# Kernel tuning notes

Hardware: AMD Instinct MI355X
Metric: run time of the kernel (lower is better)

The kernel has to match this reference:

```python
import jax, jax.numpy as jnp
import numpy as np

B, S, DIM = 32, 1, 4096
HQ, HKV, HD = 32, 8, 128
MAX_SEQ = 2048
START_POS = 2047


def _apply_rope(t, cos, sin):
    # t: [B, S, H, HD]; cos/sin: [S, HD//2]; interleaved complex rotation (Llama style)
    b, s, h, d = t.shape
    t = t.reshape(b, s, h, d // 2, 2)
    t0, t1 = t[..., 0], t[..., 1]
    c = cos[None, :, None, :]
    sn = sin[None, :, None, :]
    out = jnp.stack([t0 * c - t1 * sn, t0 * sn + t1 * c], axis=-1)
    return out.reshape(b, s, h, d)


def setup_inputs() -> dict:
    key = jax.random.key(0)
    ks = jax.random.split(key, 8)
    w_scale = 0.02
    x = jax.random.normal(ks[0], (B, S, DIM), dtype=jnp.float32)
    wq = jax.random.normal(ks[1], (HQ * HD, DIM), dtype=jnp.float32) * w_scale
    wk = jax.random.normal(ks[2], (HKV * HD, DIM), dtype=jnp.float32) * w_scale
    wv = jax.random.normal(ks[3], (HKV * HD, DIM), dtype=jnp.float32) * w_scale
    wo = jax.random.normal(ks[4], (HQ * HD, DIM), dtype=jnp.float32).T * w_scale
    wo = jnp.asarray(wo)  # [DIM, HQ*HD] as torch Linear weight [out,in]
    cache_k = jax.random.normal(ks[5], (B, MAX_SEQ, HKV, HD), dtype=jnp.float32)
    cache_v = jax.random.normal(ks[6], (B, MAX_SEQ, HKV, HD), dtype=jnp.float32)
    # rotary frequencies for the current position(s)
    inv_freq = 1.0 / (10000.0 ** (np.arange(0, HD, 2, dtype=np.float32) / HD))  # [HD//2]
    pos = np.arange(START_POS, START_POS + S, dtype=np.float32)[:, None]  # [S,1]
    ang = pos * inv_freq[None, :]
    freqs_cos = jnp.asarray(np.cos(ang), dtype=jnp.float32)
    freqs_sin = jnp.asarray(np.sin(ang), dtype=jnp.float32)
    return {"x": x, "wq": wq, "wk": wk, "wv": wv, "wo": wo,
            "cache_k": cache_k, "cache_v": cache_v,
            "freqs_cos": freqs_cos, "freqs_sin": freqs_sin,
            "start_pos": START_POS}


def reference(x, wq, wk, wv, wo, cache_k, cache_v, freqs_cos, freqs_sin, start_pos):
    b, s, dim = x.shape
    hd = 2 * freqs_cos.shape[-1]
    hq = wq.shape[0] // hd
    hkv = wk.shape[0] // hd
    n_rep = hq // hkv

    # QKV projections (torch Linear: y = x @ W.T)
    xq = (x @ wq.T).reshape(b, s, hq, hd)
    xk = (x @ wk.T).reshape(b, s, hkv, hd)
    xv = (x @ wv.T).reshape(b, s, hkv, hd)

    # RoPE on q and k
    xq = _apply_rope(xq, freqs_cos, freqs_sin)
    xk = _apply_rope(xk, freqs_cos, freqs_sin)

    # KV cache update at start_pos (static python int -> static slicing)
    ck = jax.lax.dynamic_update_slice(cache_k, xk, (0, start_pos, 0, 0))
    cv = jax.lax.dynamic_update_slice(cache_v, xv, (0, start_pos, 0, 0))
    t = start_pos + s
    keys = ck[:, :t]    # [B, T, HKV, HD]
    values = cv[:, :t]  # [B, T, HKV, HD]

    # Grouped attention without materializing repeated KV (repeat_kv fused into einsum)
    q = xq.reshape(b, s, hkv, n_rep, hd)
    scores = jnp.einsum('bsgrd,btgd->bgrst', q, keys) / jnp.sqrt(jnp.asarray(hd, x.dtype))
    attn = jax.nn.softmax(scores, axis=-1)  # decode step: attends to full history, no mask
    out = jnp.einsum('bgrst,btgd->bsgrd', attn, values).reshape(b, s, hq * hd)
    return out @ wo.T  # [B, S, DIM]
```

## Files before the change

kernel.cpp:

```cpp
#include <hip/hip_runtime.h>
#include <hip/hip_bf16.h>

typedef float vf4 __attribute__((ext_vector_type(4)));

#define B_    32
#define DIM_  4096
#define TSEQ  2048
#define LASTT 2047
#define NCH   32
#define CHUNK 64
#define CSTR  528
#define RSTR  132
#define SCL   0.08838834764831845f
#define KCH   256
#define ROWS1 6144
#define ROWS4 4096

__device__ __forceinline__ float dotv(vf4 a, vf4 b) {
    return fmaf(a[0], b[0], fmaf(a[1], b[1], fmaf(a[2], b[2], a[3] * b[3])));
}

__device__ __forceinline__ void gemm_tile_part(
    const float* __restrict__ W, const float* __restrict__ X,
    float* __restrict__ part, int rloc_base, int grow_base,
    int kb0, int kc, int rowsTot) {
    __shared__ __align__(16) vf4 wS[128][17];
    __shared__ __align__(16) vf4 xS[16][33];
    const int tid = threadIdx.x;
    const int rg = tid >> 3, bg = tid & 7;
    const int sr4 = tid >> 4, swf = tid & 15;
    const int sb = tid >> 3, sxf = tid & 7;
    float c[4][4] = {};

    for (int tile = 0; tile < 4; ++tile) {
        const int kb4 = (kb0 + tile * 64) >> 2;
        #pragma unroll
        for (int jj = 0; jj < 8; ++jj) {
            const int row = sr4 + 16 * jj;
            wS[row][swf] = __builtin_nontemporal_load(
                ((const vf4*)(W + (size_t)(rloc_base + row) * DIM_)) + kb4 + swf);
        }
        #pragma unroll
        for (int jj = 0; jj < 2; ++jj) {
            const int f4i = sxf + 8 * jj;
            xS[f4i][sb] = ((const vf4*)(X + (size_t)sb * DIM_))[kb4 + f4i];
        }
        __syncthreads();
        #pragma unroll
        for (int k4 = 0; k4 < 16; ++k4) {
            const vf4 w0 = wS[rg      ][k4];
            const vf4 w1 = wS[rg + 32 ][k4];
            const vf4 w2 = wS[rg + 64 ][k4];
            const vf4 w3 = wS[rg + 96 ][k4];
            const vf4 x0 = xS[k4][bg     ];
            const vf4 x1 = xS[k4][bg + 8 ];
            const vf4 x2 = xS[k4][bg + 16];
            const vf4 x3 = xS[k4][bg + 24];
            #pragma unroll
            for (int cm = 0; cm < 4; ++cm) {
                c[0][0] = fmaf(w0[cm], x0[cm], c[0][0]);
                c[0][1] = fmaf(w0[cm], x1[cm], c[0][1]);
                c[0][2] = fmaf(w0[cm], x2[cm], c[0][2]);
                c[0][3] = fmaf(w0[cm], x3[cm], c[0][3]);
                c[1][0] = fmaf(w1[cm], x0[cm], c[1][0]);
                c[1][1] = fmaf(w1[cm], x1[cm], c[1][1]);
                c[1][2] = fmaf(w1[cm], x2[cm], c[1][2]);
                c[1][3] = fmaf(w1[cm], x3[cm], c[1][3]);
                c[2][0] = fmaf(w2[cm], x0[cm], c[2][0]);
                c[2][1] = fmaf(w2[cm], x1[cm], c[2][1]);
                c[2][2] = fmaf(w2[cm], x2[cm], c[2][2]);
                c[2][3] = fmaf(w2[cm], x3[cm], c[2][3]);
                c[3][0] = fmaf(w3[cm], x0[cm], c[3][0]);
                c[3][1] = fmaf(w3[cm], x1[cm], c[3][1]);
                c[3][2] = fmaf(w3[cm], x2[cm], c[3][2]);
                c[3][3] = fmaf(w3[cm], x3[cm], c[3][3]);
            }
        }
        __syncthreads();
    }
    float* pb = part + (size_t)kc * rowsTot * 32;
    #pragma unroll
    for (int i = 0; i < 4; ++i)
        #pragma unroll
        for (int j = 0; j < 4; ++j)
            pb[(size_t)(grow_base + rg + 32 * i) * 32 + bg + 8 * j] = c[i][j];
}

__global__ __launch_bounds__(256) void k1_qkv(
    const float* __restrict__ x,  const float* __restrict__ wq,
    const float* __restrict__ wk, const float* __restrict__ wv,
    float* __restrict__ part) {
    const int rb = blockIdx.x >> 4, kc = blockIdx.x & 15;
    const int rbase = rb * 128;
    const float* W; int rloc;
    if (rbase < 4096)      { W = wq; rloc = rbase; }
    else if (rbase < 5120) { W = wk; rloc = rbase - 4096; }
    else                   { W = wv; rloc = rbase - 5120; }
    gemm_tile_part(W, x, part, rloc, rbase, kc * KCH, kc, ROWS1);
}

__global__ __launch_bounds__(256) void k1b_comb(
    const float* __restrict__ part, const float* __restrict__ fcos,
    const float* __restrict__ fsin, float* __restrict__ q_ws,
    float* __restrict__ k_ws, float* __restrict__ v_ws) {
    const int tid = threadIdx.x;
    const int b = tid & 31;
    const int row0 = (blockIdx.x * 8 + (tid >> 5)) * 2;
    float e = 0.f, o = 0.f;
    #pragma unroll
    for (int kc = 0; kc < 16; ++kc) {
        const float* pb = part + (size_t)kc * (ROWS1 * 32);
        e += pb[(size_t)row0 * 32 + b];
        o += pb[(size_t)(row0 + 1) * 32 + b];
    }
    if (row0 < 5120) {
        const int d = row0 & 127;
        const float cj = fcos[d >> 1], sj = fsin[d >> 1];
        const float re = e * cj - o * sj;
        const float ro = e * sj + o * cj;
        if (row0 < 4096) {
            q_ws[(size_t)b * 4096 + row0]     = re * SCL;
            q_ws[(size_t)b * 4096 + row0 + 1] = ro * SCL;
        } else {
            k_ws[(size_t)b * 1024 + row0 - 4096] = re;
            k_ws[(size_t)b * 1024 + row0 - 4095] = ro;
        }
    } else {
        v_ws[(size_t)b * 1024 + row0 - 5120] = e;
        v_ws[(size_t)b * 1024 + row0 - 5119] = o;
    }
}

__global__ __launch_bounds__(64) void k2_attn(
    const float* __restrict__ q_ws, const float* __restrict__ k_ws,
    const float* __restrict__ v_ws, const float* __restrict__ cK,
    const float* __restrict__ cV,   float* __restrict__ cws) {
    __shared__ float p_lds[4][64];
    const int blk = blockIdx.x;
    const int b = blk >> 8, g = (blk >> 5) & 7, c = blk & 31;
    const int lane = threadIdx.x & 63;
    const int tbase = c * CHUNK;
    const int s = lane & 7, pown = lane >> 3;

    const vf4* qb4 = (const vf4*)(q_ws + ((size_t)b * 32 + g * 4) * 128);
    vf4 q4[4][4];
    #pragma unroll
    for (int r = 0; r < 4; ++r)
        #pragma unroll
        for (int j = 0; j < 4; ++j)
            q4[r][j] = qb4[r * 32 + j * 8 + s];

    const vf4* kwsrow = (const vf4*)(k_ws + ((size_t)b * 8 + g) * 128);
    const vf4* vwsrow = (const vf4*)(v_ws + ((size_t)b * 8 + g) * 128);

    vf4 kb[4];
    {
        const int t = tbase + pown;
        const vf4* kr = (t == LASTT) ? kwsrow
            : (const vf4*)(cK + (((size_t)b * TSEQ + t) * 8 + g) * 128);
        #pragma unroll
        for (int j = 0; j < 4; ++j)
            kb[j] = __builtin_nontemporal_load(&kr[j * 8 + s]);
    }
    #pragma unroll
    for (int pg = 0; pg < 8; ++pg) {
        vf4 kn[4];
        if (pg < 7) {
            const int t = tbase + (pg + 1) * 8 + pown;
            const vf4* kr = (t == LASTT) ? kwsrow
                : (const vf4*)(cK + (((size_t)b * TSEQ + t) * 8 + g) * 128);
            #pragma unroll
            for (int j = 0; j < 4; ++j)
                kn[j] = __builtin_nontemporal_load(&kr[j * 8 + s]);
        }
        float a0 = 0.f, a1 = 0.f, a2 = 0.f, a3 = 0.f;
        #pragma unroll
        for (int j = 0; j < 4; ++j) {
            a0 += dotv(q4[0][j], kb[j]);
            a1 += dotv(q4[1][j], kb[j]);
            a2 += dotv(q4[2][j], kb[j]);
            a3 += dotv(q4[3][j], kb[j]);
        }
        #pragma unroll
        for (int m = 4; m >= 1; m >>= 1) {
            a0 += __shfl_xor(a0, m); a1 += __shfl_xor(a1, m);
            a2 += __shfl_xor(a2, m); a3 += __shfl_xor(a3, m);
        }
        const int idx = pg * 8 + pown;
        if (s == 0) p_lds[0][idx] = a0;
        if (s == 1) p_lds[1][idx] = a1;
        if (s == 2) p_lds[2][idx] = a2;
        if (s == 3) p_lds[3][idx] = a3;
        #pragma unroll
        for (int j = 0; j < 4; ++j) kb[j] = kn[j];
    }
    __syncthreads();

    const int h = lane >> 5, col = lane & 31;
    vf4 vb;
    {
        const int t = tbase + h;
        const vf4* vp = (t == LASTT) ? vwsrow
            : (const vf4*)(cV + (((size_t)b * TSEQ + t) * 8 + g) * 128);
        vb = __builtin_nontemporal_load(&vp[col]);
    }

    float sc[4], M[4], S[4];
    #pragma unroll
    for (int r = 0; r < 4; ++r) sc[r] = p_lds[r][lane];
    #pragma unroll
    for (int r = 0; r < 4; ++r) {
        float m = sc[r];
        #pragma unroll
        for (int msk = 32; msk >= 1; msk >>= 1) m = fmaxf(m, __shfl_xor(m, msk));
        M[r] = m;
        const float p = __expf(sc[r] - m);
        p_lds[r][lane] = p;
        float su = p;
        #pragma unroll
        for (int msk = 32; msk >= 1; msk >>= 1) su += __shfl_xor(su, msk);
        S[r] = su;
    }
    __syncthreads();

    float a[4][4] = {};
    #pragma unroll 8
    for (int tt = 0; tt < 32; ++tt) {
        vf4 vn;
        if (tt < 31) {
            const int t = tbase + (tt + 1) * 2 + h;
            const vf4* vp = (t == LASTT) ? vwsrow
                : (const vf4*)(cV + (((size_t)b * TSEQ + t) * 8 + g) * 128);
            vn = __builtin_nontemporal_load(&vp[col]);
        }
        #pragma unroll
        for (int r = 0; r < 4; ++r) {
            const float pr = p_lds[r][tt * 2 + h];
            a[r][0] = fmaf(pr, vb[0], a[r][0]);
            a[r][1] = fmaf(pr, vb[1], a[r][1]);
            a[r][2] = fmaf(pr, vb[2], a[r][2]);
            a[r][3] = fmaf(pr, vb[3], a[r][3]);
        }
        vb = vn;
    }
    #pragma unroll
    for (int r = 0; r < 4; ++r)
        #pragma unroll
        for (int j = 0; j < 4; ++j) a[r][j] += __shfl_xor(a[r][j], 32);

    float* base = cws + (size_t)blk * CSTR;
    if (lane < 32) {
        #pragma unroll
        for (int r = 0; r < 4; ++r) {
            vf4 v; v[0] = a[r][0]; v[1] = a[r][1]; v[2] = a[r][2]; v[3] = a[r][3];
            *(vf4*)(base + r * RSTR + col * 4) = v;
        }
    }
    if (lane == 0) {
        #pragma unroll
        for (int r = 0; r < 4; ++r) {
            base[r * RSTR + 128] = M[r];
            base[r * RSTR + 129] = S[r];
        }
    }
}

__global__ __launch_bounds__(256) void k3_comb(const float* __restrict__ cws,
                                               float* __restrict__ attn) {
    const int blk = blockIdx.x;
    const int b = blk >> 3, g = blk & 7;
    const int tid = threadIdx.x, r = tid >> 6, lane = tid & 63;
    const float* base0 = cws + (size_t)blk * 32 * CSTR + r * RSTR;
    float mi[32], si[32];
    float Mg = -3.4e38f;
    #pragma unroll
    for (int ci = 0; ci < 32; ++ci) {
        mi[ci] = base0[(size_t)ci * CSTR + 128];
        si[ci] = base0[(size_t)ci * CSTR + 129];
        Mg = fmaxf(Mg, mi[ci]);
    }
    float w[32], Sg = 0.f;
    #pragma unroll
    for (int ci = 0; ci < 32; ++ci) {
        w[ci] = __expf(mi[ci] - Mg);
        Sg = fmaf(si[ci], w[ci], Sg);
    }
    const float inv = 1.f / Sg;
    #pragma unroll
    for (int dd = 0; dd < 2; ++dd) {
        const int d = lane + dd * 64;
        float o = 0.f;
        #pragma unroll
        for (int ci = 0; ci < 32; ++ci)
            o = fmaf(base0[(size_t)ci * CSTR + d], w[ci], o);
        attn[((size_t)b * 32 + g * 4 + r) * 128 + d] = o * inv;
    }
}

__global__ __launch_bounds__(256) void k4_out(
    const float* __restrict__ attn, const float* __restrict__ wo,
    float* __restrict__ part) {
    const int rb = blockIdx.x >> 4, kc = blockIdx.x & 15;
    const int rbase = rb * 128;
    gemm_tile_part(wo, attn, part, rbase, rbase, kc * KCH, kc, ROWS4);
}

__global__ __launch_bounds__(256) void k4b_comb(const float* __restrict__ part,
                                                float* __restrict__ out) {
    const int tid = threadIdx.x;
    const int b = tid & 31;
    const int row = blockIdx.x * 8 + (tid >> 5);
    float acc = 0.f;
    #pragma unroll
    for (int kc = 0; kc < 16; ++kc)
        acc += part[(size_t)kc * (ROWS4 * 32) + (size_t)row * 32 + b];
    out[(size_t)b * 4096 + row] = acc;
}

extern "C" void kernel_launch(void* const* d_in, const int* in_sizes, int n_in,
                              void* d_out, int out_size, void* d_ws, size_t ws_size,
                              hipStream_t stream) {
    const float* x    = (const float*)d_in[0];
    const float* wq   = (const float*)d_in[1];
    const float* wk   = (const float*)d_in[2];
    const float* wv   = (const float*)d_in[3];
    const float* wo   = (const float*)d_in[4];
    const float* cK   = (const float*)d_in[5];
    const float* cV   = (const float*)d_in[6];
    const float* fcos = (const float*)d_in[7];
    const float* fsin = (const float*)d_in[8];
    float* ws   = (float*)d_ws;
    float* A    = ws;
    float* q_ws = ws + 4325376;
    float* k_ws = ws + 4456448;
    float* v_ws = ws + 4489216;
    float* attn = ws + 4521984;
    float* out  = (float*)d_out;

    hipLaunchKernelGGL(k1_qkv,   dim3(768),  dim3(256), 0, stream,
                       x, wq, wk, wv, A);
    hipLaunchKernelGGL(k1b_comb, dim3(384),  dim3(256), 0, stream,
                       A, fcos, fsin, q_ws, k_ws, v_ws);
    hipLaunchKernelGGL(k2_attn,  dim3(8192), dim3(64),  0, stream,
                       q_ws, k_ws, v_ws, cK, cV, A);
    hipLaunchKernelGGL(k3_comb,  dim3(256),  dim3(256), 0, stream, A, attn);
    hipLaunchKernelGGL(k4_out,   dim3(512),  dim3(256), 0, stream, attn, wo, A);
    hipLaunchKernelGGL(k4b_comb, dim3(512),  dim3(256), 0, stream, A, out);
}
```

Baseline: 186.8 us.

## Restructure attention split: per-batch chunk blocks covering all KV heads with contiguous rows

The attention kernel now launches one 256-thread block per batch and 128-token chunk, where each wave walks 32 tokens and lanes split across all 8 KV heads. Each K/V cache row is therefore read as one contiguous 4 KB segment instead of per-head strided pieces. Softmax partials are reduced across waves in LDS, and a single record per (batch, chunk) is written, which halves the number of partials the combine kernel merges. Separately, the weight loads in the GEMM tile drop the nontemporal hint. The costs are more LDS, extra barriers and fewer, larger blocks (512 instead of 8192).

```diff
diff --git a/kernel.cpp b/kernel.cpp
--- a/kernel.cpp
+++ b/kernel.cpp
@@ -7,14 +7,11 @@
 #define DIM_  4096
 #define TSEQ  2048
 #define LASTT 2047
-#define NCH   32
-#define CHUNK 64
-#define CSTR  528
-#define RSTR  132
 #define SCL   0.08838834764831845f
 #define KCH   256
 #define ROWS1 6144
 #define ROWS4 4096
+#define RECF  4224
 
 __device__ __forceinline__ float dotv(vf4 a, vf4 b) {
     return fmaf(a[0], b[0], fmaf(a[1], b[1], fmaf(a[2], b[2], a[3] * b[3])));
@@ -37,8 +34,8 @@
         #pragma unroll
         for (int jj = 0; jj < 8; ++jj) {
             const int row = sr4 + 16 * jj;
-            wS[row][swf] = __builtin_nontemporal_load(
-                ((const vf4*)(W + (size_t)(rloc_base + row) * DIM_)) + kb4 + swf);
+            wS[row][swf] =
+                ((const vf4*)(W + (size_t)(rloc_base + row) * DIM_))[kb4 + swf];
         }
         #pragma unroll
         for (int jj = 0; jj < 2; ++jj) {
@@ -131,16 +128,20 @@
     }
 }
 
-__global__ __launch_bounds__(64) void k2_attn(
+__global__ __launch_bounds__(256) void k2_attn(
     const float* __restrict__ q_ws, const float* __restrict__ k_ws,
     const float* __restrict__ v_ws, const float* __restrict__ cK,
     const float* __restrict__ cV,   float* __restrict__ cws) {
-    __shared__ float p_lds[4][64];
+    __shared__ float p_lds[8][4][129];
+    __shared__ __align__(16) float pacc[4][8][132];
+    __shared__ float wred[4][32];
+    __shared__ float wsum[4][32];
+    __shared__ float mM[32];
     const int blk = blockIdx.x;
-    const int b = blk >> 8, g = (blk >> 5) & 7, c = blk & 31;
-    const int lane = threadIdx.x & 63;
-    const int tbase = c * CHUNK;
-    const int s = lane & 7, pown = lane >> 3;
+    const int b = blk >> 4, ch = blk & 15;
+    const int tid = threadIdx.x, wave = tid >> 6, lane = tid & 63;
+    const int g = lane >> 3, s = lane & 7;
+    const int tb = ch * 128 + wave * 32;
 
     const vf4* qb4 = (const vf4*)(q_ws + ((size_t)b * 32 + g * 4) * 128);
     vf4 q4[4][4];
@@ -155,18 +156,18 @@
 
     vf4 kb[4];
     {
-        const int t = tbase + pown;
+        const int t = tb;
         const vf4* kr = (t == LASTT) ? kwsrow
             : (const vf4*)(cK + (((size_t)b * TSEQ + t) * 8 + g) * 128);
         #pragma unroll
         for (int j = 0; j < 4; ++j)
             kb[j] = __builtin_nontemporal_load(&kr[j * 8 + s]);
     }
-    #pragma unroll
-    for (int pg = 0; pg < 8; ++pg) {
+    #pragma unroll 4
+    for (int tt = 0; tt < 32; ++tt) {
         vf4 kn[4];
-        if (pg < 7) {
-            const int t = tbase + (pg + 1) * 8 + pown;
+        if (tt < 31) {
+            const int t = tb + tt + 1;
             const vf4* kr = (t == LASTT) ? kwsrow
                 : (const vf4*)(cK + (((size_t)b * TSEQ + t) * 8 + g) * 128);
             #pragma unroll
@@ -186,81 +187,95 @@
             a0 += __shfl_xor(a0, m); a1 += __shfl_xor(a1, m);
             a2 += __shfl_xor(a2, m); a3 += __shfl_xor(a3, m);
         }
-        const int idx = pg * 8 + pown;
-        if (s == 0) p_lds[0][idx] = a0;
-        if (s == 1) p_lds[1][idx] = a1;
-        if (s == 2) p_lds[2][idx] = a2;
-        if (s == 3) p_lds[3][idx] = a3;
+        const float val = (s == 0) ? a0 : (s == 1) ? a1 : (s == 2) ? a2 : a3;
+        if (s < 4) p_lds[g][s][wave * 32 + tt] = val;
         #pragma unroll
         for (int j = 0; j < 4; ++j) kb[j] = kn[j];
     }
+
+    const int pr_ = lane & 31, g2 = pr_ >> 2, r2 = pr_ & 3;
+    float m = -3.4e38f;
+    #pragma unroll 8
+    for (int tt = 0; tt < 32; ++tt)
+        m = fmaxf(m, p_lds[g2][r2][wave * 32 + tt]);
+    float su = 0.f;
+    #pragma unroll 8
+    for (int tt = 0; tt < 32; ++tt)
+        su += __expf(p_lds[g2][r2][wave * 32 + tt] - m);
+    if (lane < 32) { wred[wave][pr_] = m; wsum[wave][pr_] = su; }
     __syncthreads();
-
-    const int h = lane >> 5, col = lane & 31;
-    vf4 vb;
+    if (tid < 32) {
+        float M = fmaxf(fmaxf(wred[0][tid], wred[1][tid]),
+                        fmaxf(wred[2][tid], wred[3][tid]));
+        float S = wsum[0][tid] * __expf(wred[0][tid] - M)
+                + wsum[1][tid] * __expf(wred[1][tid] - M)
+                + wsum[2][tid] * __expf(wred[2][tid] - M)
+                + wsum[3][tid] * __expf(wred[3][tid] - M);
+        mM[tid] = M;
+        float* rec = cws + (size_t)blk * RECF + (tid >> 2) * 528 + (tid & 3) * 132;
+        rec[128] = M;
+        rec[129] = S;
+    }
+    __syncthreads();
+
+    #pragma unroll
+    for (int i = 0; i < 16; ++i) {
+        const int idx = i * 64 + lane;
+        const int t5 = idx & 31, rr = (idx >> 5) & 3, gg = idx >> 7;
+        const float v = p_lds[gg][rr][wave * 32 + t5];
+        p_lds[gg][rr][wave * 32 + t5] = __expf(v - mM[(gg << 2) | rr]);
+    }
+
+    vf4 a[4][4];
+    #pragma unroll
+    for (int r = 0; r < 4; ++r)
+        #pragma unroll
+        for (int j = 0; j < 4; ++j)
+            a[r][j] = (vf4){0.f, 0.f, 0.f, 0.f};
+    vf4 vb[4];
     {
-        const int t = tbase + h;
+        const int t = tb;
         const vf4* vp = (t == LASTT) ? vwsrow
             : (const vf4*)(cV + (((size_t)b * TSEQ + t) * 8 + g) * 128);
-        vb = __builtin_nontemporal_load(&vp[col]);
-    }
-
-    float sc[4], M[4], S[4];
-    #pragma unroll
-    for (int r = 0; r < 4; ++r) sc[r] = p_lds[r][lane];
-    #pragma unroll
-    for (int r = 0; r < 4; ++r) {
-        float m = sc[r];
-        #pragma unroll
-        for (int msk = 32; msk >= 1; msk >>= 1) m = fmaxf(m, __shfl_xor(m, msk));
-        M[r] = m;
-        const float p = __expf(sc[r] - m);
-        p_lds[r][lane] = p;
-        float su = p;
-        #pragma unroll
-        for (int msk = 32; msk >= 1; msk >>= 1) su += __shfl_xor(su, msk);
-        S[r] = su;
-    }
-    __syncthreads();
-
-    float a[4][4] = {};
-    #pragma unroll 8
+        #pragma unroll
+        for (int j = 0; j < 4; ++j)
+            vb[j] = __builtin_nontemporal_load(&vp[j * 8 + s]);
+    }
+    #pragma unroll 4
     for (int tt = 0; tt < 32; ++tt) {
-        vf4 vn;
+        vf4 vn[4];
         if (tt < 31) {
-            const int t = tbase + (tt + 1) * 2 + h;
+            const int t = tb + tt + 1;
             const vf4* vp = (t == LASTT) ? vwsrow
                 : (const vf4*)(cV + (((size_t)b * TSEQ + t) * 8 + g) * 128);
-            vn = __builtin_nontemporal_load(&vp[col]);
+            #pragma unroll
+            for (int j = 0; j < 4; ++j)
+                vn[j] = __builtin_nontemporal_load(&vp[j * 8 + s]);
         }
         #pragma unroll
         for (int r = 0; r < 4; ++r) {
-            const float pr = p_lds[r][tt * 2 + h];
-            a[r][0] = fmaf(pr, vb[0], a[r][0]);
-            a[r][1] = fmaf(pr, vb[1], a[r][1]);
-            a[r][2] = fmaf(pr, vb[2], a[r][2]);
-            a[r][3] = fmaf(pr, vb[3], a[r][3]);
-        }
-        vb = vn;
-    }
-    #pragma unroll
-    for (int r = 0; r < 4; ++r)
-        #pragma unroll
-        for (int j = 0; j < 4; ++j) a[r][j] += __shfl_xor(a[r][j], 32);
-
-    float* base = cws + (size_t)blk * CSTR;
-    if (lane < 32) {
-        #pragma unroll
-        for (int r = 0; r < 4; ++r) {
-            vf4 v; v[0] = a[r][0]; v[1] = a[r][1]; v[2] = a[r][2]; v[3] = a[r][3];
-            *(vf4*)(base + r * RSTR + col * 4) = v;
-        }
-    }
-    if (lane == 0) {
-        #pragma unroll
-        for (int r = 0; r < 4; ++r) {
-            base[r * RSTR + 128] = M[r];
-            base[r * RSTR + 129] = S[r];
+            const float pw = p_lds[g][r][wave * 32 + tt];
+            #pragma unroll
+            for (int j = 0; j < 4; ++j)
+                a[r][j] += pw * vb[j];
+        }
+        #pragma unroll
+        for (int j = 0; j < 4; ++j) vb[j] = vn[j];
+    }
+
+    float* recb = cws + (size_t)blk * RECF;
+    #pragma unroll
+    for (int r = 0; r < 4; ++r) {
+        __syncthreads();
+        #pragma unroll
+        for (int j = 0; j < 4; ++j)
+            *(vf4*)&pacc[wave][g][(j * 8 + s) * 4] = a[r][j];
+        __syncthreads();
+        for (int idx = tid; idx < 1024; idx += 256) {
+            const int gg = idx >> 7, d = idx & 127;
+            const float sum = pacc[0][gg][d] + pacc[1][gg][d]
+                            + pacc[2][gg][d] + pacc[3][gg][d];
+            recb[gg * 528 + r * 132 + d] = sum;
         }
     }
 }
@@ -270,18 +285,18 @@
     const int blk = blockIdx.x;
     const int b = blk >> 3, g = blk & 7;
     const int tid = threadIdx.x, r = tid >> 6, lane = tid & 63;
-    const float* base0 = cws + (size_t)blk * 32 * CSTR + r * RSTR;
-    float mi[32], si[32];
+    const float* base0 = cws + (size_t)b * 16 * RECF + g * 528 + r * 132;
+    float mi[16], si[16];
     float Mg = -3.4e38f;
     #pragma unroll
-    for (int ci = 0; ci < 32; ++ci) {
-        mi[ci] = base0[(size_t)ci * CSTR + 128];
-        si[ci] = base0[(size_t)ci * CSTR + 129];
+    for (int ci = 0; ci < 16; ++ci) {
+        mi[ci] = base0[(size_t)ci * RECF + 128];
+        si[ci] = base0[(size_t)ci * RECF + 129];
         Mg = fmaxf(Mg, mi[ci]);
     }
-    float w[32], Sg = 0.f;
-    #pragma unroll
-    for (int ci = 0; ci < 32; ++ci) {
+    float w[16], Sg = 0.f;
+    #pragma unroll
+    for (int ci = 0; ci < 16; ++ci) {
         w[ci] = __expf(mi[ci] - Mg);
         Sg = fmaf(si[ci], w[ci], Sg);
     }
@@ -291,8 +306,8 @@
         const int d = lane + dd * 64;
         float o = 0.f;
         #pragma unroll
-        for (int ci = 0; ci < 32; ++ci)
-            o = fmaf(base0[(size_t)ci * CSTR + d], w[ci], o);
+        for (int ci = 0; ci < 16; ++ci)
+            o = fmaf(base0[(size_t)ci * RECF + d], w[ci], o);
         attn[((size_t)b * 32 + g * 4 + r) * 128 + d] = o * inv;
     }
 }
@@ -331,17 +346,17 @@
     const float* fsin = (const float*)d_in[8];
     float* ws   = (float*)d_ws;
     float* A    = ws;
-    float* q_ws = ws + 4325376;
-    float* k_ws = ws + 4456448;
-    float* v_ws = ws + 4489216;
-    float* attn = ws + 4521984;
+    float* q_ws = ws + 3145728;
+    float* k_ws = ws + 3276800;
+    float* v_ws = ws + 3309568;
+    float* attn = ws + 3342336;
     float* out  = (float*)d_out;
 
     hipLaunchKernelGGL(k1_qkv,   dim3(768),  dim3(256), 0, stream,
                        x, wq, wk, wv, A);
     hipLaunchKernelGGL(k1b_comb, dim3(384),  dim3(256), 0, stream,
                        A, fcos, fsin, q_ws, k_ws, v_ws);
-    hipLaunchKernelGGL(k2_attn,  dim3(8192), dim3(64),  0, stream,
+    hipLaunchKernelGGL(k2_attn,  dim3(512),  dim3(256), 0, stream,
                        q_ws, k_ws, v_ws, cK, cV, A);
     hipLaunchKernelGGL(k3_comb,  dim3(256),  dim3(256), 0, stream, A, attn);
     hipLaunchKernelGGL(k4_out,   dim3(512),  dim3(256), 0, stream, attn, wo, A);
```

New measurement: 170.9 us. 8.5% less time.
